# Kernel tuning notes

Measured on AMD Instinct MI355X. Metric: run time of the kernel, lower is better.

Reference implementation:

```python
import jax, jax.numpy as jnp
import numpy as np
from jax import lax


def setup_inputs() -> dict:
    key = jax.random.key(0)
    kx, kih, khh, kb = jax.random.split(key, 4)
    B, T, I, H = 32, 512, 1024, 1024
    s_ih = 1.0 / np.sqrt(I)
    s_hh = 1.0 / np.sqrt(H)
    return {
        "x": jax.random.normal(kx, (B, T, I), dtype=jnp.float32),
        "W_ih": jax.random.normal(kih, (4 * H, I), dtype=jnp.float32) * s_ih,
        "W_hh": jax.random.normal(khh, (4 * H, H), dtype=jnp.float32) * s_hh,
        "b": jax.random.normal(kb, (4 * H,), dtype=jnp.float32) * s_hh,
    }


def reference(x, W_ih, W_hh, b):
    # x: [B, T, I]; LSTM with gate order i, f, g, o (equinox LSTMCell).
    B, T, I = x.shape
    H = W_hh.shape[1]
    # Precompute the input projection for all timesteps (same math, hoisted).
    xW = jnp.einsum("bti,gi->btg", x, W_ih) + b  # [B, T, 4H]
    xW_t = jnp.transpose(xW, (1, 0, 2))          # [T, B, 4H]

    h0 = jnp.zeros((B, H), dtype=x.dtype)
    c0 = jnp.zeros((B, H), dtype=x.dtype)

    def step(carry, xt):
        h, c = carry
        z = xt + h @ W_hh.T                      # [B, 4H]
        i, f, g, o = jnp.split(z, 4, axis=-1)
        i = jax.nn.sigmoid(i)
        f = jax.nn.sigmoid(f)
        g = jnp.tanh(g)
        o = jax.nn.sigmoid(o)
        c = f * c + i * g
        h = o * jnp.tanh(c)
        return (h, c), h

    _, hs = lax.scan(step, (h0, c0), xW_t)       # hs: [T, B, H]
    return jnp.transpose(hs, (1, 0, 2))          # [B, T, H]
```

## Files before the change

kernel.cpp:

```cpp
#include <hip/hip_runtime.h>
#include <stdint.h>

#define BB 32
#define TT 512
#define KK 1024
#define GG 4096
#define MM 16384
#define NSLICE 32
#define SCAN_WGS 64
#define HPAD 1032

typedef __attribute__((ext_vector_type(8))) short short8;
typedef __attribute__((ext_vector_type(4))) short short4v;
typedef __attribute__((ext_vector_type(4))) float f32x4;
typedef unsigned long long u64;

__device__ inline short f2bf(float f) {
  union { float f; unsigned u; } v; v.f = f;
  unsigned r = (v.u + 0x7FFFu + ((v.u >> 16) & 1u)) >> 16;
  return (short)(unsigned short)r;
}
__device__ inline float bf2f(short s) {
  union { unsigned u; float f; } v; v.u = ((unsigned)(unsigned short)s) << 16;
  return v.f;
}
__device__ inline float sigmoid_f(float x) { return 1.0f / (1.0f + __expf(-x)); }
__device__ inline float tanh_f(float x)    { return 1.0f - 2.0f / (__expf(2.0f * x) + 1.0f); }


__global__ void zero_ws(unsigned* __restrict__ p, int n) {
  int i = blockIdx.x * 256 + threadIdx.x;
  if (i < n) p[i] = 0u;
}

__global__ void cvt_bf16(const float* __restrict__ in, short* __restrict__ out, int n4) {
  int i = blockIdx.x * 256 + threadIdx.x;
  if (i >= n4) return;
  f32x4 v = *(const f32x4*)(in + (size_t)i * 4);
  short4v o;
  o.x = f2bf(v.x); o.y = f2bf(v.y); o.z = f2bf(v.z); o.w = f2bf(v.w);
  *(short4v*)(out + (size_t)i * 4) = o;
}

__global__ void pack_whh(const float* __restrict__ Whh, short* __restrict__ wpack) {
  int idx = blockIdx.x * 256 + threadIdx.x;
  if (idx >= NSLICE * 8 * 32 * 64) return;
  int lane  = idx & 63;
  int s     = (idx >> 6) & 31;
  int nt    = (idx >> 11) & 7;
  int slice = idx >> 14;
  int c     = lane & 15;
  int row   = (c & 3) * 1024 + slice * 32 + nt * 4 + (c >> 2);
  int k     = s * 32 + (lane >> 4) * 8;
  const float* src = Whh + (size_t)row * KK + k;
  short8 v;
#pragma unroll
  for (int j = 0; j < 8; ++j) v[j] = f2bf(src[j]);
  *(short8*)(wpack + ((size_t)((slice * 8 + nt) * 32 + s)) * 512 + lane * 8) = v;
}

template <bool XWF32>
__global__ __launch_bounds__(256) void gemm_xw(const short* __restrict__ A,
                                               const short* __restrict__ Bw,
                                               const float* __restrict__ bias,
                                               void* __restrict__ Cv) {
  __shared__ short As[128 * 32];
  __shared__ short Bs[128 * 32];
  const int tid = threadIdx.x;
  const int m0 = blockIdx.y * 128;
  const int n0 = blockIdx.x * 128;
  const int lane = tid & 63, wv = tid >> 6;
  const int wm = (wv >> 1) * 64, wn = (wv & 1) * 64;
  const int fr = lane & 15;
  const int fq = (lane >> 4) * 8;
  const int quad = lane >> 4;
  f32x4 acc[4][4];
#pragma unroll
  for (int i = 0; i < 4; ++i)
#pragma unroll
    for (int j = 0; j < 4; ++j) acc[i][j] = (f32x4){0.f, 0.f, 0.f, 0.f};

  const int sr = tid >> 2;
  const int sc = (tid & 3) * 8;
  const short* Ag = A + (size_t)(m0 + sr) * KK + sc;
  const short* Bg = Bw + (size_t)(n0 + sr) * KK + sc;

  for (int kb = 0; kb < KK; kb += 32) {
    short8 a0 = *(const short8*)(Ag + kb);
    short8 a1 = *(const short8*)(Ag + (size_t)64 * KK + kb);
    short8 b0 = *(const short8*)(Bg + kb);
    short8 b1 = *(const short8*)(Bg + (size_t)64 * KK + kb);
    __syncthreads();
    *(short8*)&As[sr * 32 + sc] = a0;
    *(short8*)&As[(64 + sr) * 32 + sc] = a1;
    *(short8*)&Bs[sr * 32 + sc] = b0;
    *(short8*)&Bs[(64 + sr) * 32 + sc] = b1;
    __syncthreads();
    short8 af[4], bf[4];
#pragma unroll
    for (int i = 0; i < 4; ++i) {
      af[i] = *(const short8*)&As[(wm + i * 16 + fr) * 32 + fq];
      bf[i] = *(const short8*)&Bs[(wn + i * 16 + fr) * 32 + fq];
    }
#pragma unroll
    for (int i = 0; i < 4; ++i)
#pragma unroll
      for (int j = 0; j < 4; ++j)
        acc[i][j] = __builtin_amdgcn_mfma_f32_16x16x32_bf16(af[i], bf[j], acc[i][j], 0, 0, 0);
  }
#pragma unroll
  for (int i = 0; i < 4; ++i) {
    int mrow = m0 + wm + i * 16 + quad * 4;
#pragma unroll
    for (int j = 0; j < 4; ++j) {
      int ncol = n0 + wn + j * 16 + fr;
      float bv = bias[ncol];
#pragma unroll
      for (int r = 0; r < 4; ++r) {
        float v = acc[i][j][r] + bv;
        size_t idx = (size_t)(mrow + r) * GG + ncol;
        if (XWF32) ((float*)Cv)[idx] = v;
        else       ((short*)Cv)[idx] = f2bf(v);
      }
    }
  }
}

template <bool XWF32>
__global__ __launch_bounds__(512, 2) void lstm_scan(const void* __restrict__ xWv,
                                                    const short* __restrict__ wpack,
                                                    short* __restrict__ hbuf,
                                                    unsigned* __restrict__ flags,
                                                    float* __restrict__ out) {
  const int wg = blockIdx.x;
  const int group = wg >> 5;
  const int slice = wg & 31;
  const int tid = threadIdx.x;
  const int lane = tid & 63;
  const int wv = tid >> 6;
  const int quad = lane >> 4;
  const int bloc = lane & 15;
  const int bglob = group * 16 + bloc;
  const int jglob = slice * 32 + wv * 4 + quad;

  short8 wreg[32];
  {
    const short* wp = wpack + ((size_t)((slice * 8 + wv) * 32)) * 512 + lane * 8;
#pragma unroll
    for (int s = 0; s < 32; ++s) wreg[s] = *(const short8*)(wp + (size_t)s * 512);
  }

  __shared__ short hstage[16 * HPAD];

  float c_reg = 0.f;
  const float* xwf = (const float*)xWv;
  const short* xwh = (const short*)xWv;

  float xwv_[4];
  {
    size_t xb = ((size_t)bglob * TT) * GG + jglob;
#pragma unroll
    for (int g = 0; g < 4; ++g)
      xwv_[g] = XWF32 ? xwf[xb + (size_t)g * 1024] : bf2f(xwh[xb + (size_t)g * 1024]);
  }

  unsigned* gflags = flags + (size_t)group * 32 * 16;

#pragma unroll 1
  for (int t = 0; t < TT; ++t) {
    const int buf = t & 1;
    float xwn[4] = {0.f, 0.f, 0.f, 0.f};
    if (t + 1 < TT) {
      size_t xb = ((size_t)bglob * TT + t + 1) * GG + jglob;
#pragma unroll
      for (int g = 0; g < 4; ++g)
        xwn[g] = XWF32 ? xwf[xb + (size_t)g * 1024] : bf2f(xwh[xb + (size_t)g * 1024]);
    }

    if (wv == 0 && t > 0) {
      const unsigned need = (unsigned)t;
      while (true) {
        unsigned f = need;
        if (lane < 32)
          f = __hip_atomic_load(&gflags[(size_t)lane * 16], __ATOMIC_RELAXED,
                                __HIP_MEMORY_SCOPE_AGENT);
        if (__all((int)(f >= need))) break;
        __builtin_amdgcn_s_sleep(1);
      }
    }
    __syncthreads();

    const u64* sb = (const u64*)(hbuf + ((size_t)(buf * 2 + group)) * 16384);
    u64 hv[8];
#pragma unroll
    for (int k = 0; k < 8; ++k) {
      int pos = k * 64 + lane;
      int row = pos >> 5, cu = pos & 31;
      hv[k] = __hip_atomic_load(&sb[row * 256 + wv * 32 + cu], __ATOMIC_RELAXED,
                                __HIP_MEMORY_SCOPE_AGENT);
    }
#pragma unroll
    for (int k = 0; k < 8; ++k) {
      int pos = k * 64 + lane;
      int row = pos >> 5, cu = pos & 31;
      *(u64*)&hstage[row * HPAD + (wv * 32 + cu) * 4] = hv[k];
    }
    __syncthreads();

    f32x4 acc0 = (f32x4){0.f, 0.f, 0.f, 0.f};
    f32x4 acc1 = (f32x4){0.f, 0.f, 0.f, 0.f};
    const short* hrow = hstage + bloc * HPAD + quad * 8;
#pragma unroll
    for (int s = 0; s < 32; s += 2) {
      short8 b0 = *(const short8*)(hrow + s * 32);
      short8 b1 = *(const short8*)(hrow + (s + 1) * 32);
      acc0 = __builtin_amdgcn_mfma_f32_16x16x32_bf16(wreg[s], b0, acc0, 0, 0, 0);
      acc1 = __builtin_amdgcn_mfma_f32_16x16x32_bf16(wreg[s + 1], b1, acc1, 0, 0, 0);
    }

    float i_ = sigmoid_f(acc0[0] + acc1[0] + xwv_[0]);
    float f_ = sigmoid_f(acc0[1] + acc1[1] + xwv_[1]);
    float g_ = tanh_f(acc0[2] + acc1[2] + xwv_[2]);
    float o_ = sigmoid_f(acc0[3] + acc1[3] + xwv_[3]);
    c_reg = f_ * c_reg + i_ * g_;
    float h_ = o_ * tanh_f(c_reg);

    unsigned hb16 = (unsigned)(unsigned short)f2bf(h_);
    unsigned oth = __shfl_xor(hb16, 16, 64);
    if (!(quad & 1)) {
      unsigned packed = hb16 | (oth << 16);
      size_t so = ((size_t)((buf ^ 1) * 2 + group)) * 16384 +
                  (size_t)bloc * 1024 + jglob;
      __hip_atomic_store((unsigned*)(hbuf + so), packed, __ATOMIC_RELAXED,
                         __HIP_MEMORY_SCOPE_AGENT);
    }

    __syncthreads();
    if (tid == 0)
      __hip_atomic_store(&flags[(size_t)wg * 16], (unsigned)(t + 1),
                         __ATOMIC_RELAXED, __HIP_MEMORY_SCOPE_AGENT);

    out[((size_t)bglob * TT + t) * 1024 + jglob] = h_;

#pragma unroll
    for (int g = 0; g < 4; ++g) xwv_[g] = xwn[g];
  }
}


extern "C" void kernel_launch(void* const* d_in, const int* in_sizes, int n_in,
                              void* d_out, int out_size, void* d_ws, size_t ws_size,
                              hipStream_t stream) {
  const float* x    = (const float*)d_in[0];
  const float* Wih  = (const float*)d_in[1];
  const float* Whh  = (const float*)d_in[2];
  const float* bias = (const float*)d_in[3];
  float* out = (float*)d_out;

  char* ws = (char*)d_ws;
  const size_t o_xbf   = 0;
  const size_t o_wih   = 33554432;
  const size_t o_wpack = 41943040;
  const size_t o_hbuf  = 50331648;
  const size_t o_flag  = 50462720;
  const size_t o_xw    = 50466816;
  const bool xwf32 = ws_size >= (o_xw + (size_t)MM * GG * 4);

  short* xbf      = (short*)(ws + o_xbf);
  short* wihbf    = (short*)(ws + o_wih);
  short* wpack    = (short*)(ws + o_wpack);
  short* hbuf     = (short*)(ws + o_hbuf);
  unsigned* flags = (unsigned*)(ws + o_flag);
  void* xw        = (void*)(ws + o_xw);

  zero_ws<<<132, 256, 0, stream>>>((unsigned*)(ws + o_hbuf), 33792);
  cvt_bf16<<<16384, 256, 0, stream>>>(x, xbf, 4194304);
  cvt_bf16<<<4096, 256, 0, stream>>>(Wih, wihbf, 1048576);
  pack_whh<<<2048, 256, 0, stream>>>(Whh, wpack);

  dim3 g1(GG / 128, MM / 128);
  if (xwf32) gemm_xw<true ><<<g1, 256, 0, stream>>>(xbf, wihbf, bias, xw);
  else       gemm_xw<false><<<g1, 256, 0, stream>>>(xbf, wihbf, bias, xw);

  if (xwf32) lstm_scan<true ><<<SCAN_WGS, 512, 0, stream>>>(xw, wpack, hbuf, flags, out);
  else       lstm_scan<false><<<SCAN_WGS, 512, 0, stream>>>(xw, wpack, hbuf, flags, out);
}
```

Before: 2.361 ms.

## Replace per-step all-slice barrier with per-wave producer flags plus read-done flags

Splits the single per-step completion flag into a data-ready flag and a read-done flag. Each wave now waits only on the four producer workgroups whose h slices it actually loads, instead of one wave waiting on all 32 and then a block-wide barrier. Wave 0 also waits until every workgroup has finished reading the previous buffer before overwriting it. The aim is to shorten the serial dependency chain between timesteps. In exchange there is more flag polling traffic and an extra flag store per step, and the double-buffer safety now rests on the new read-done protocol.

```diff
diff --git a/kernel.cpp b/kernel.cpp
--- a/kernel.cpp
+++ b/kernel.cpp
@@ -130,7 +130,8 @@
 __global__ __launch_bounds__(512, 2) void lstm_scan(const void* __restrict__ xWv,
                                                     const short* __restrict__ wpack,
                                                     short* __restrict__ hbuf,
-                                                    unsigned* __restrict__ flags,
+                                                    unsigned* __restrict__ dataf,
+                                                    unsigned* __restrict__ readf,
                                                     float* __restrict__ out) {
   const int wg = blockIdx.x;
   const int group = wg >> 5;
@@ -164,7 +165,8 @@
       xwv_[g] = XWF32 ? xwf[xb + (size_t)g * 1024] : bf2f(xwh[xb + (size_t)g * 1024]);
   }
 
-  unsigned* gflags = flags + (size_t)group * 32 * 16;
+  unsigned* gdataf = dataf + (size_t)group * 32 * 16;
+  unsigned* greadf = readf + (size_t)group * 32 * 16;
 
 #pragma unroll 1
   for (int t = 0; t < TT; ++t) {
@@ -177,18 +179,34 @@
         xwn[g] = XWF32 ? xwf[xb + (size_t)g * 1024] : bf2f(xwh[xb + (size_t)g * 1024]);
     }
 
-    if (wv == 0 && t > 0) {
+    if (t > 0) {
       const unsigned need = (unsigned)t;
-      while (true) {
-        unsigned f = need;
-        if (lane < 32)
-          f = __hip_atomic_load(&gflags[(size_t)lane * 16], __ATOMIC_RELAXED,
-                                __HIP_MEMORY_SCOPE_AGENT);
-        if (__all((int)(f >= need))) break;
-        __builtin_amdgcn_s_sleep(1);
+      if (wv == 0) {
+        while (true) {
+          unsigned ok = 1u;
+          if (lane < 32) {
+            unsigned f = __hip_atomic_load(&greadf[(size_t)lane * 16],
+                                           __ATOMIC_RELAXED, __HIP_MEMORY_SCOPE_AGENT);
+            ok = (f >= need);
+          } else if (lane < 36) {
+            unsigned f = __hip_atomic_load(&gdataf[(size_t)(lane - 32) * 16],
+                                           __ATOMIC_RELAXED, __HIP_MEMORY_SCOPE_AGENT);
+            ok = (f >= need);
+          }
+          if (__all((int)ok)) break;
+          __builtin_amdgcn_s_sleep(1);
+        }
+      } else {
+        while (true) {
+          unsigned f = need;
+          if (lane < 4)
+            f = __hip_atomic_load(&gdataf[(size_t)(wv * 4 + lane) * 16],
+                                  __ATOMIC_RELAXED, __HIP_MEMORY_SCOPE_AGENT);
+          if (__all((int)(f >= need))) break;
+          __builtin_amdgcn_s_sleep(1);
+        }
       }
     }
-    __syncthreads();
 
     const u64* sb = (const u64*)(hbuf + ((size_t)(buf * 2 + group)) * 16384);
     u64 hv[8];
@@ -206,6 +224,10 @@
       *(u64*)&hstage[row * HPAD + (wv * 32 + cu) * 4] = hv[k];
     }
     __syncthreads();
+
+    if (tid == 0)
+      __hip_atomic_store(&readf[(size_t)wg * 16], (unsigned)(t + 1),
+                         __ATOMIC_RELAXED, __HIP_MEMORY_SCOPE_AGENT);
 
     f32x4 acc0 = (f32x4){0.f, 0.f, 0.f, 0.f};
     f32x4 acc1 = (f32x4){0.f, 0.f, 0.f, 0.f};
@@ -237,7 +259,7 @@
 
     __syncthreads();
     if (tid == 0)
-      __hip_atomic_store(&flags[(size_t)wg * 16], (unsigned)(t + 1),
+      __hip_atomic_store(&dataf[(size_t)wg * 16], (unsigned)(t + 1),
                          __ATOMIC_RELAXED, __HIP_MEMORY_SCOPE_AGENT);
 
     out[((size_t)bglob * TT + t) * 1024 + jglob] = h_;
@@ -262,18 +284,20 @@
   const size_t o_wih   = 33554432;
   const size_t o_wpack = 41943040;
   const size_t o_hbuf  = 50331648;
-  const size_t o_flag  = 50462720;
-  const size_t o_xw    = 50466816;
+  const size_t o_dataf = 50462720;
+  const size_t o_readf = 50466816;
+  const size_t o_xw    = 50470912;
   const bool xwf32 = ws_size >= (o_xw + (size_t)MM * GG * 4);
 
   short* xbf      = (short*)(ws + o_xbf);
   short* wihbf    = (short*)(ws + o_wih);
   short* wpack    = (short*)(ws + o_wpack);
   short* hbuf     = (short*)(ws + o_hbuf);
-  unsigned* flags = (unsigned*)(ws + o_flag);
+  unsigned* dataf = (unsigned*)(ws + o_dataf);
+  unsigned* readf = (unsigned*)(ws + o_readf);
   void* xw        = (void*)(ws + o_xw);
 
-  zero_ws<<<132, 256, 0, stream>>>((unsigned*)(ws + o_hbuf), 33792);
+  zero_ws<<<136, 256, 0, stream>>>((unsigned*)(ws + o_hbuf), 34816);
   cvt_bf16<<<16384, 256, 0, stream>>>(x, xbf, 4194304);
   cvt_bf16<<<4096, 256, 0, stream>>>(Wih, wihbf, 1048576);
   pack_whh<<<2048, 256, 0, stream>>>(Whh, wpack);
@@ -282,6 +306,6 @@
   if (xwf32) gemm_xw<true ><<<g1, 256, 0, stream>>>(xbf, wihbf, bias, xw);
   else       gemm_xw<false><<<g1, 256, 0, stream>>>(xbf, wihbf, bias, xw);
 
-  if (xwf32) lstm_scan<true ><<<SCAN_WGS, 512, 0, stream>>>(xw, wpack, hbuf, flags, out);
-  else       lstm_scan<false><<<SCAN_WGS, 512, 0, stream>>>(xw, wpack, hbuf, flags, out);
-}
+  if (xwf32) lstm_scan<true ><<<SCAN_WGS, 512, 0, stream>>>(xw, wpack, hbuf, dataf, readf, out);
+  else       lstm_scan<false><<<SCAN_WGS, 512, 0, stream>>>(xw, wpack, hbuf, dataf, readf, out);
+}
```

New measurement: 2.358 ms. No clear change (-0.1%).
